# Optimization experiments

Measured on AMD Instinct MI355X. Metric: run time of the kernel, lower is better.

The kernel has to match this reference:

```python
import jax, jax.numpy as jnp
import numpy as np

H_BANDWIDTH = 0.5
EPS = 1e-5


def setup_inputs() -> dict:
    key = jax.random.key(0)
    k1, k2 = jax.random.split(key)
    x = jax.random.normal(k1, (4, 256, 64, 64), dtype=jnp.float32)
    y = jax.random.normal(k2, (4, 256, 64, 64), dtype=jnp.float32)
    return {"x": x, "y": y}


def reference(x, y):
    # x, y: (N, C, H, W), H=W=64 so no pooling branch is taken
    N, C, H, W = x.shape
    # mean over batch and spatial dims of y -> per-channel mu, shape (1, C, 1, 1)
    y_mu = jnp.mean(y, axis=(0, 2, 3)).reshape(1, C, 1, 1)
    x_c = x - y_mu
    y_c = y - y_mu
    # L2-normalize over channel dim
    x_n = x_c / jnp.linalg.norm(x_c, axis=1, keepdims=True)
    y_n = y_c / jnp.linalg.norm(y_c, axis=1, keepdims=True)
    x_n = x_n.reshape(N, C, H * W)
    y_n = y_n.reshape(N, C, H * W)
    # cosine similarity: (N, HW, HW)
    cos = jnp.einsum("ncp,ncq->npq", x_n, y_n)
    d = 1.0 - cos
    d_min = jnp.min(d, axis=2, keepdims=True)
    d_tilde = d / (d_min + EPS)
    w = jnp.exp((1.0 - d_tilde) / H_BANDWIDTH)
    cx_ij = w / jnp.sum(w, axis=2, keepdims=True)
    cx = jnp.mean(jnp.max(cx_ij, axis=1), axis=1)  # (N,)
    cx_loss = jnp.mean(-jnp.log(cx + EPS))
    return cx_loss
```

## Files before the change

### kernel.cpp

```cpp
#include <hip/hip_runtime.h>
#include <hip/hip_bf16.h>

typedef short bf16x8 __attribute__((ext_vector_type(8)));
typedef float f32x4 __attribute__((ext_vector_type(4)));

#define NB 4
#define C 256
#define HW 4096
#define NROWS (NB * HW)
#define EPSF 1e-5f

__device__ __forceinline__ unsigned short f2bf(float f) {
    unsigned int u = __float_as_uint(f);
    unsigned int r = u + 0x7fffu + ((u >> 16) & 1u);
    return (unsigned short)(r >> 16);
}
__device__ __forceinline__ float bf2f(unsigned int h) {
    return __uint_as_float(h << 16);
}
__device__ __forceinline__ void unpack8(uint4 u, float* v) {
    unsigned int w0 = u.x, w1 = u.y, w2 = u.z, w3 = u.w;
    v[0] = bf2f(w0 & 0xffffu); v[1] = bf2f(w0 >> 16);
    v[2] = bf2f(w1 & 0xffffu); v[3] = bf2f(w1 >> 16);
    v[4] = bf2f(w2 & 0xffffu); v[5] = bf2f(w2 >> 16);
    v[6] = bf2f(w3 & 0xffffu); v[7] = bf2f(w3 >> 16);
}
__device__ __forceinline__ float waveReduceSum(float v) {
    for (int off = 32; off > 0; off >>= 1) v += __shfl_xor(v, off);
    return v;
}
typedef __attribute__((address_space(1))) const unsigned int glb_cu;
typedef __attribute__((address_space(3))) unsigned int lds_u;
__device__ __forceinline__ void async_copy16(const unsigned short* g, unsigned short* l) {
    __builtin_amdgcn_global_load_lds((glb_cu*)g, (lds_u*)l, 16, 0, 0);
}

__global__ __launch_bounds__(256) void mu_kernel(const float* __restrict__ y,
                                                 float* __restrict__ mu,
                                                 float* __restrict__ cxsum,
                                                 unsigned int* __restrict__ ticket) {
    int c = blockIdx.x;
    int tid = threadIdx.x;
    if (c == 0) {
        if (tid < NB) cxsum[tid] = 0.f;
        if (tid == NB) *ticket = 0u;
    }
    float s = 0.f;
    const float* base = y + (size_t)c * HW;
    for (int n = 0; n < NB; n++) {
        const float* bn = base + (size_t)n * C * HW;
        for (int i = tid; i < HW; i += 256) s += bn[i];
    }
    s = waveReduceSum(s);
    __shared__ float red[4];
    int lane = tid & 63, wave = tid >> 6;
    if (lane == 0) red[wave] = s;
    __syncthreads();
    if (tid == 0) mu[c] = (red[0] + red[1] + red[2] + red[3]) * (1.0f / 16384.0f);
}

#define TP 32
#define TSTRIDE 257
__global__ __launch_bounds__(256) void prep_kernel(const float* __restrict__ x,
                                                   const float* __restrict__ y,
                                                   const float* __restrict__ mu,
                                                   unsigned short* __restrict__ Xn,
                                                   unsigned short* __restrict__ Yn) {
    __shared__ float smu[C];
    __shared__ float tile[TP * TSTRIDE];
    __shared__ float red[8 * 32];
    __shared__ float invn[TP];
    int tid = threadIdx.x;
    smu[tid] = mu[tid];
    int blk = blockIdx.x;
    int n = blk >> 7;
    int p0 = (blk & 127) * TP;
    int tp = tid & 31, cc = tid >> 5;
    __syncthreads();
    for (int pass = 0; pass < 2; pass++) {
        const float* in = pass ? y : x;
        unsigned short* out = pass ? Yn : Xn;
        const float* base = in + (size_t)n * C * HW + p0 + tp;
        float ssq = 0.f;
        for (int c = cc; c < C; c += 8) {
            float v = base[(size_t)c * HW] - smu[c];
            tile[tp * TSTRIDE + c] = v;
            ssq += v * v;
        }
        red[cc * 32 + tp] = ssq;
        __syncthreads();
        if (tid < 32) {
            float s = 0.f;
            for (int k = 0; k < 8; k++) s += red[k * 32 + tid];
            invn[tid] = rsqrtf(s);
        }
        __syncthreads();
        int c2 = (tid & 127) * 2;
        int pp = tid >> 7;
        for (int p = pp; p < TP; p += 2) {
            float inv = invn[p];
            unsigned short b0 = f2bf(tile[p * TSTRIDE + c2] * inv);
            unsigned short b1 = f2bf(tile[p * TSTRIDE + c2 + 1] * inv);
            unsigned int pack = (unsigned int)b0 | ((unsigned int)b1 << 16);
            ((unsigned int*)out)[(size_t)(n * HW + p0 + p) * (C / 2) + (c2 >> 1)] = pack;
        }
        __syncthreads();
    }
}

#define EPSTRIDE 136
#define STAGE(s, b)                                                            \
    do {                                                                       \
        unsigned short* lA = lds_us + (b) * 16384;                             \
        unsigned short* lB = lds_us + (b) * 16384 + 8192;                      \
        _Pragma("unroll")                                                      \
        for (int t = 0; t < 4; t++) {                                          \
            int slot = t * 256 + tid;                                          \
            int r = slot >> 3, cl = slot & 7;                                  \
            int c = (s) * 8 + (cl ^ (r & 7));                                  \
            async_copy16(Ab + (size_t)r * C + c * 8, lA + slot * 8);           \
        }                                                                      \
        _Pragma("unroll")                                                      \
        for (int t = 0; t < 4; t++) {                                          \
            int slot = t * 256 + tid;                                          \
            int r = slot >> 3, cl = slot & 7;                                  \
            int c = (s) * 8 + (cl ^ (r & 7));                                  \
            async_copy16(Bb + (size_t)r * C + c * 8, lB + slot * 8);           \
        }                                                                      \
    } while (0)

#define COMPUTE(b)                                                             \
    do {                                                                       \
        const unsigned short* lA = lds_us + (b) * 16384;                       \
        const unsigned short* lB = lds_us + (b) * 16384 + 8192;                \
        _Pragma("unroll")                                                      \
        for (int kkl = 0; kkl < 2; kkl++) {                                    \
            int cl4 = kkl * 4 + quad;                                          \
            int clp = cl4 ^ (mrow & 7);                                        \
            bf16x8 af[4], bfr[4];                                              \
            _Pragma("unroll")                                                  \
            for (int i = 0; i < 4; i++) {                                      \
                af[i]  = *(const bf16x8*)(lA + (wm + i * 16 + mrow) * 64 + clp * 8); \
                bfr[i] = *(const bf16x8*)(lB + (wn + i * 16 + mrow) * 64 + clp * 8); \
            }                                                                  \
            _Pragma("unroll")                                                  \
            for (int i = 0; i < 4; i++)                                        \
                _Pragma("unroll")                                              \
                for (int j = 0; j < 4; j++)                                    \
                    acc[i][j] = __builtin_amdgcn_mfma_f32_16x16x32_bf16(af[i], bfr[j], acc[i][j], 0, 0, 0); \
        }                                                                      \
    } while (0)

__global__ __launch_bounds__(256, 2) void gemm_cos(const unsigned short* __restrict__ Xn,
                                                   const unsigned short* __restrict__ Yn,
                                                   unsigned short* __restrict__ Cos) {
    __shared__ unsigned short lds_us[32768];
    int n = blockIdx.z;
    int pBase = blockIdx.y * 128, qBase = blockIdx.x * 128;
    const unsigned short* Ab = Xn + ((size_t)n * HW + pBase) * C;
    const unsigned short* Bb = Yn + ((size_t)n * HW + qBase) * C;
    int tid = threadIdx.x, lane = tid & 63, wave = tid >> 6;
    int wm = (wave >> 1) * 64, wn = (wave & 1) * 64;
    int mrow = lane & 15, quad = lane >> 4;

    f32x4 acc[4][4];
#pragma unroll
    for (int i = 0; i < 4; i++)
#pragma unroll
        for (int j = 0; j < 4; j++) acc[i][j] = (f32x4){0.f, 0.f, 0.f, 0.f};

    STAGE(0, 0);
    __syncthreads();

#pragma unroll
    for (int s = 0; s < 3; s++) {
        STAGE(s + 1, (s + 1) & 1);
        __builtin_amdgcn_sched_barrier(0);
        COMPUTE(s & 1);
        __syncthreads();
    }

    COMPUTE(1);
    __syncthreads();

    unsigned short* epb = lds_us;
    int col = lane & 15, quad4 = quad * 4;
#pragma unroll
    for (int i = 0; i < 4; i++)
#pragma unroll
        for (int j = 0; j < 4; j++)
#pragma unroll
            for (int r = 0; r < 4; r++)
                epb[(wm + i * 16 + quad4 + r) * EPSTRIDE + wn + j * 16 + col] = f2bf(acc[i][j][r]);
    __syncthreads();
    unsigned short* Crow = Cos + (size_t)n * HW * HW;
#pragma unroll
    for (int it = 0; it < 8; it++) {
        int e = it * 2048 + tid * 8;
        int r = e >> 7, cg = e & 127;
        uint4 o = *(const uint4*)(epb + r * EPSTRIDE + cg);
        *(uint4*)(Crow + (size_t)(pBase + r) * HW + qBase + cg) = o;
    }
}

__global__ __launch_bounds__(256, 3) void rowcol(const unsigned short* __restrict__ Cos,
                                                 unsigned short* __restrict__ partial) {
    int n = blockIdx.y, chunk = blockIdx.x;
    int tid = threadIdx.x, lane = tid & 63, wave = tid >> 6;
    const unsigned short* rowbase = Cos + ((size_t)n * HW + chunk * 8) * HW;
    __shared__ float redm[8][4];
    __shared__ float sval[8][4];

    uint4 d[8][2];
#pragma unroll
    for (int r = 0; r < 8; r++) {
        const unsigned short* rp = rowbase + (size_t)r * HW;
        d[r][0] = *(const uint4*)(rp + tid * 8);
        d[r][1] = *(const uint4*)(rp + 2048 + tid * 8);
    }

    float m8[8];
#pragma unroll
    for (int r = 0; r < 8; r++) {
        float v[16];
        unpack8(d[r][0], v); unpack8(d[r][1], v + 8);
        float m = v[0];
#pragma unroll
        for (int k = 1; k < 16; k++) m = fmaxf(m, v[k]);
        m8[r] = m;
    }
#pragma unroll
    for (int off = 32; off > 0; off >>= 1)
#pragma unroll
        for (int r = 0; r < 8; r++) m8[r] = fmaxf(m8[r], __shfl_xor(m8[r], off));
    if (lane == 0)
#pragma unroll
        for (int r = 0; r < 8; r++) redm[r][wave] = m8[r];
    __syncthreads();

    float alpha[8], basec[8];
#pragma unroll
    for (int r = 0; r < 8; r++) {
        float M = fmaxf(fmaxf(redm[r][0], redm[r][1]), fmaxf(redm[r][2], redm[r][3]));
        alpha[r] = 2.0f / ((1.0f - M) + EPSF);
        basec[r] = 2.0f - alpha[r];
    }

    float s8[8];
#pragma unroll
    for (int r = 0; r < 8; r++) {
        float v[16];
        unpack8(d[r][0], v); unpack8(d[r][1], v + 8);
        float s = 0.f;
#pragma unroll
        for (int k = 0; k < 16; k++) s += __expf(fmaf(alpha[r], v[k], basec[r]));
        s8[r] = s;
    }
#pragma unroll
    for (int off = 32; off > 0; off >>= 1)
#pragma unroll
        for (int r = 0; r < 8; r++) s8[r] += __shfl_xor(s8[r], off);
    if (lane == 0)
#pragma unroll
        for (int r = 0; r < 8; r++) sval[r][wave] = s8[r];
    __syncthreads();

    float cmax[16];
#pragma unroll
    for (int k = 0; k < 16; k++) cmax[k] = -1e30f;
#pragma unroll
    for (int r = 0; r < 8; r++) {
        float S = sval[r][0] + sval[r][1] + sval[r][2] + sval[r][3];
        float beta = basec[r] - __logf(S);
        float v[16];
        unpack8(d[r][0], v); unpack8(d[r][1], v + 8);
#pragma unroll
        for (int k = 0; k < 16; k++) cmax[k] = fmaxf(cmax[k], fmaf(alpha[r], v[k], beta));
    }

    unsigned short* outp = partial + ((size_t)(n * 512 + chunk)) * HW;
    uint4 o0, o1;
    o0.x = (unsigned int)f2bf(cmax[0]) | ((unsigned int)f2bf(cmax[1]) << 16);
    o0.y = (unsigned int)f2bf(cmax[2]) | ((unsigned int)f2bf(cmax[3]) << 16);
    o0.z = (unsigned int)f2bf(cmax[4]) | ((unsigned int)f2bf(cmax[5]) << 16);
    o0.w = (unsigned int)f2bf(cmax[6]) | ((unsigned int)f2bf(cmax[7]) << 16);
    o1.x = (unsigned int)f2bf(cmax[8]) | ((unsigned int)f2bf(cmax[9]) << 16);
    o1.y = (unsigned int)f2bf(cmax[10]) | ((unsigned int)f2bf(cmax[11]) << 16);
    o1.z = (unsigned int)f2bf(cmax[12]) | ((unsigned int)f2bf(cmax[13]) << 16);
    o1.w = (unsigned int)f2bf(cmax[14]) | ((unsigned int)f2bf(cmax[15]) << 16);
    *(uint4*)(outp + tid * 8) = o0;
    *(uint4*)(outp + 2048 + tid * 8) = o1;
}

__global__ __launch_bounds__(256) void colred(const unsigned short* __restrict__ partial,
                                              float* __restrict__ cxsum,
                                              unsigned int* __restrict__ ticket,
                                              float* __restrict__ out) {
    int n = blockIdx.y, g = blockIdx.x;
    int tid = threadIdx.x;
    int qi = tid & 63, cs = tid >> 6;
    const unsigned short* p = partial + ((size_t)(n * 512 + cs)) * HW + g * 64 + qi;
    float m = -1e30f;
#pragma unroll 8
    for (int c = cs; c < 512; c += 4) {
        m = fmaxf(m, bf2f(*p));
        p += (size_t)4 * HW;
    }
    __shared__ float sm[4][64];
    sm[cs][qi] = m;
    __syncthreads();
    if (tid < 64) {
        float mm = fmaxf(fmaxf(sm[0][qi], sm[1][qi]), fmaxf(sm[2][qi], sm[3][qi]));
        float s = __expf(mm);
        s = waveReduceSum(s);
        if (qi == 0) {
            atomicAdd(&cxsum[n], s);
            __threadfence();
            unsigned int old = atomicAdd(ticket, 1u);
            if (old == (unsigned int)(64 * NB - 1)) {
                __threadfence();
                float loss = 0.f;
                for (int b = 0; b < NB; b++) {
                    float csn = atomicAdd(&cxsum[b], 0.0f);
                    loss += -logf(csn * (1.0f / 4096.0f) + EPSF);
                }
                out[0] = loss * 0.25f;
            }
        }
    }
}

extern "C" void kernel_launch(void* const* d_in, const int* in_sizes, int n_in,
                              void* d_out, int out_size, void* d_ws, size_t ws_size,
                              hipStream_t stream) {
    const float* x = (const float*)d_in[0];
    const float* y = (const float*)d_in[1];
    float* out = (float*)d_out;
    char* ws = (char*)d_ws;

    float* mu               = (float*)(ws + 0);
    float* cxsum            = (float*)(ws + 1024);
    unsigned int* ticket    = (unsigned int*)(ws + 1040);
    unsigned short* Xn      = (unsigned short*)(ws + 2097152);
    unsigned short* Yn      = (unsigned short*)(ws + 10485760);
    unsigned short* partial = (unsigned short*)(ws + 2097152);
    unsigned short* Cos     = (unsigned short*)(ws + 18874368);

    mu_kernel<<<C, 256, 0, stream>>>(y, mu, cxsum, ticket);
    prep_kernel<<<NROWS / TP, 256, 0, stream>>>(x, y, mu, Xn, Yn);
    gemm_cos<<<dim3(HW / 128, HW / 128, NB), 256, 0, stream>>>(Xn, Yn, Cos);
    rowcol<<<dim3(512, NB), 256, 0, stream>>>(Cos, partial);
    colred<<<dim3(64, NB), 256, 0, stream>>>(partial, cxsum, ticket, out);
}
```

Before: 203.3 us.

## Process batches sequentially to keep cosine matrix cache-resident; vectorize colred loads

The GEMM and row/column reduction kernels now run once per batch element in a host loop, reusing a single 32 MB cosine buffer instead of writing a 128 MB tensor for all batches. The smaller intermediate is meant to stay in the large last-level cache between the GEMM write and the rowcol read. Because later GEMM passes still read Xn, the partial buffer moves to its own region so it no longer overwrites Xn. colred now loads 8 bf16 values per thread with uint4 loads and reduces across 32 slices in shared memory. The trade-off is more kernel launches, each with a smaller grid.

```diff
diff --git a/kernel.cpp b/kernel.cpp
--- a/kernel.cpp
+++ b/kernel.cpp
@@ -153,9 +153,9 @@
 
 __global__ __launch_bounds__(256, 2) void gemm_cos(const unsigned short* __restrict__ Xn,
                                                    const unsigned short* __restrict__ Yn,
-                                                   unsigned short* __restrict__ Cos) {
+                                                   unsigned short* __restrict__ Cos,
+                                                   int n) {
     __shared__ unsigned short lds_us[32768];
-    int n = blockIdx.z;
     int pBase = blockIdx.y * 128, qBase = blockIdx.x * 128;
     const unsigned short* Ab = Xn + ((size_t)n * HW + pBase) * C;
     const unsigned short* Bb = Yn + ((size_t)n * HW + qBase) * C;
@@ -193,7 +193,7 @@
             for (int r = 0; r < 4; r++)
                 epb[(wm + i * 16 + quad4 + r) * EPSTRIDE + wn + j * 16 + col] = f2bf(acc[i][j][r]);
     __syncthreads();
-    unsigned short* Crow = Cos + (size_t)n * HW * HW;
+    unsigned short* Crow = Cos;
 #pragma unroll
     for (int it = 0; it < 8; it++) {
         int e = it * 2048 + tid * 8;
@@ -204,10 +204,11 @@
 }
 
 __global__ __launch_bounds__(256, 3) void rowcol(const unsigned short* __restrict__ Cos,
-                                                 unsigned short* __restrict__ partial) {
-    int n = blockIdx.y, chunk = blockIdx.x;
+                                                 unsigned short* __restrict__ partial,
+                                                 int n) {
+    int chunk = blockIdx.x;
     int tid = threadIdx.x, lane = tid & 63, wave = tid >> 6;
-    const unsigned short* rowbase = Cos + ((size_t)n * HW + chunk * 8) * HW;
+    const unsigned short* rowbase = Cos + ((size_t)chunk * 8) * HW;
     __shared__ float redm[8][4];
     __shared__ float sval[8][4];
 
@@ -298,23 +299,33 @@
                                               float* __restrict__ out) {
     int n = blockIdx.y, g = blockIdx.x;
     int tid = threadIdx.x;
-    int qi = tid & 63, cs = tid >> 6;
-    const unsigned short* p = partial + ((size_t)(n * 512 + cs)) * HW + g * 64 + qi;
-    float m = -1e30f;
-#pragma unroll 8
-    for (int c = cs; c < 512; c += 4) {
-        m = fmaxf(m, bf2f(*p));
-        p += (size_t)4 * HW;
-    }
-    __shared__ float sm[4][64];
-    sm[cs][qi] = m;
+    int qo = tid & 7;
+    int cs = tid >> 3;
+    const unsigned short* p = partial + ((size_t)(n * 512 + cs)) * HW + g * 64 + qo * 8;
+    float mx[8];
+#pragma unroll
+    for (int k = 0; k < 8; k++) mx[k] = -1e30f;
+#pragma unroll 4
+    for (int c = cs; c < 512; c += 32) {
+        uint4 u = *(const uint4*)p;
+        float v[8];
+        unpack8(u, v);
+#pragma unroll
+        for (int k = 0; k < 8; k++) mx[k] = fmaxf(mx[k], v[k]);
+        p += (size_t)32 * HW;
+    }
+    __shared__ float sm[32][64];
+#pragma unroll
+    for (int k = 0; k < 8; k++) sm[cs][qo * 8 + k] = mx[k];
     __syncthreads();
     if (tid < 64) {
-        float mm = fmaxf(fmaxf(sm[0][qi], sm[1][qi]), fmaxf(sm[2][qi], sm[3][qi]));
-        float s = __expf(mm);
-        s = waveReduceSum(s);
-        if (qi == 0) {
-            atomicAdd(&cxsum[n], s);
+        float mm = -1e30f;
+#pragma unroll
+        for (int s = 0; s < 32; s++) mm = fmaxf(mm, sm[s][tid]);
+        float sv = __expf(mm);
+        sv = waveReduceSum(sv);
+        if (tid == 0) {
+            atomicAdd(&cxsum[n], sv);
             __threadfence();
             unsigned int old = atomicAdd(ticket, 1u);
             if (old == (unsigned int)(64 * NB - 1)) {
@@ -344,11 +355,15 @@
     unsigned short* Xn      = (unsigned short*)(ws + 2097152);
     unsigned short* Yn      = (unsigned short*)(ws + 10485760);
     unsigned short* partial = (unsigned short*)(ws + 2097152);
-    unsigned short* Cos     = (unsigned short*)(ws + 18874368);
+    unsigned short* Cos     = (unsigned short*)(ws + 52428800);
+
+    partial = (unsigned short*)(ws + 18874368);
 
     mu_kernel<<<C, 256, 0, stream>>>(y, mu, cxsum, ticket);
     prep_kernel<<<NROWS / TP, 256, 0, stream>>>(x, y, mu, Xn, Yn);
-    gemm_cos<<<dim3(HW / 128, HW / 128, NB), 256, 0, stream>>>(Xn, Yn, Cos);
-    rowcol<<<dim3(512, NB), 256, 0, stream>>>(Cos, partial);
+    for (int n = 0; n < NB; n++) {
+        gemm_cos<<<dim3(HW / 128, HW / 128), 256, 0, stream>>>(Xn, Yn, Cos, n);
+        rowcol<<<512, 256, 0, stream>>>(Cos, partial, n);
+    }
     colred<<<dim3(64, NB), 256, 0, stream>>>(partial, cxsum, ticket, out);
 }
```

Measured after the change: 221.2 us. 8.8% more time.
